# Kernel optimization log

Hardware: AMD Instinct MI355X
Metric: run time of the kernel (lower is better)

## Reference

```python
import jax, jax.numpy as jnp
import numpy as np

B, T, D = 2, 4096, 1024
H = 8
HD = D // H            # head_dim = 128
STRIDES = (1, 1, 2, 2, 4, 4, 8, 8)   # resolution_schedule
BANDS = 8              # spectral_bands
RH = 256               # router_hidden


def setup_inputs() -> dict:
    key = jax.random.key(0)
    ks = jax.random.split(key, 12)
    def xavier(k, shape):
        fan_in, fan_out = shape[-2], shape[-1]
        lim = 0.5 * (6.0 / (fan_in + fan_out)) ** 0.5   # gain=0.5 xavier_uniform
        return jax.random.uniform(k, shape, jnp.float32, -lim, lim)
    return {
        "x":          jax.random.normal(ks[0], (B, T, D), jnp.float32),
        "Wq":         xavier(ks[1], (H, D, HD)),
        "Wk":         xavier(ks[2], (H, D, HD)),
        "Wv":         xavier(ks[3], (H, D, HD)),
        "band_gates": jax.random.normal(ks[4], (H, BANDS), jnp.float32) * 0.1,
        "alphas":     jax.random.normal(ks[5], (H,), jnp.float32) * 0.1,
        "rW1":        xavier(ks[6], (D, RH)),
        "rb1":        jnp.zeros((RH,), jnp.float32),
        "rW2":        xavier(ks[7], (RH, H)),
        "rb2":        jnp.zeros((H,), jnp.float32),
        "Wout":       xavier(ks[8], (HD, D)),
    }


def _flux_head(x, Wq, Wk, Wv, band_gate, alpha, stride):
    # one FluxHead: strided K/V pooling + spectral logit gating + contra-flow residual
    q = jnp.einsum('btd,dh->bth', x, Wq)          # [B,T,HD]
    k = jnp.einsum('btd,dh->bth', x, Wk)
    v = jnp.einsum('btd,dh->bth', x, Wv)
    Tk = T // stride
    k = k.reshape(B, Tk, stride, HD).mean(axis=2)  # avg-pool K/V along time
    v = v.reshape(B, Tk, stride, HD).mean(axis=2)
    logits = jnp.einsum('bth,bkh->btk', q, k) / jnp.sqrt(jnp.float32(HD))  # [B,T,Tk]
    # spectral frequency gating on logits (rFFT over key axis, per-band sigmoid gain)
    F = jnp.fft.rfft(logits, axis=-1)              # [B,T,Tk//2+1] complex
    nbins = F.shape[-1]
    band_idx = jnp.clip((jnp.arange(nbins) * BANDS) // nbins, 0, BANDS - 1)
    gains = jax.nn.sigmoid(band_gate)[band_idx]    # [nbins]
    logits = jnp.fft.irfft(F * gains, n=Tk, axis=-1)
    attn = jax.nn.softmax(logits, axis=-1)
    out = jnp.einsum('btk,bkh->bth', attn, v)      # [B,T,HD]
    # contra-flow: reverse-sequence residual with learned gate
    return out + jnp.tanh(alpha) * out[:, ::-1, :]


def reference(x, Wq, Wk, Wv, band_gates, alphas, rW1, rb1, rW2, rb2, Wout):
    head_outs = [
        _flux_head(x, Wq[h], Wk[h], Wv[h], band_gates[h], alphas[h], STRIDES[h])
        for h in range(H)
    ]
    stacked = jnp.stack(head_outs, axis=2)                      # [B,T,H,HD]
    hid = jax.nn.relu(jnp.einsum('btd,dr->btr', x, rW1) + rb1)  # router MLP
    w = jax.nn.softmax(jnp.einsum('btr,rh->bth', hid, rW2) + rb2, axis=-1)
    mixed = jnp.einsum('bth,bthc->btc', w, stacked)             # [B,T,HD]
    return jnp.einsum('btc,cd->btd', mixed, Wout)               # [B,T,D]
```

## Files before the change

kernel.cpp:

```cpp
#include <hip/hip_runtime.h>
#include <hip/hip_bf16.h>

typedef __attribute__((ext_vector_type(8))) short short8;
typedef __attribute__((ext_vector_type(4))) short short4v;
typedef __attribute__((ext_vector_type(4))) float f32x4;
typedef unsigned short u16;

#define T_ 4096
#define D_ 1024
#define ISSL2E (0.08838834764831845f * 1.4426950408889634f)

__device__ __forceinline__ u16 f2bf(float f) {
  union { float f; unsigned u; } v; v.f = f;
  unsigned r = v.u + 0x7FFFu + ((v.u >> 16) & 1u);
  return (u16)(r >> 16);
}

__global__ __launch_bounds__(256) void prep_all(const float* __restrict__ x,
    const float* __restrict__ Wq, const float* __restrict__ Wk, const float* __restrict__ Wv,
    const float* __restrict__ rW1, const float* __restrict__ Wout,
    u16* __restrict__ p1, u16* __restrict__ p2, u16* __restrict__ p4, u16* __restrict__ p8,
    u16* __restrict__ wqT, u16* __restrict__ kvT, u16* __restrict__ rw1T, u16* __restrict__ woutT) {
  const int blk = blockIdx.x;
  if (blk < 1024) {
    const int b = blk >> 9, t0 = (blk & 511) << 3;
    const float* src = x + ((long)b * T_ + t0) * D_;
#pragma unroll
    for (int j = 0; j < 4; ++j) {
      const int c = threadIdx.x + j * 256;
      float v[8];
#pragma unroll
      for (int r = 0; r < 8; ++r) v[r] = src[r * D_ + c];
#pragma unroll
      for (int r = 0; r < 8; ++r) p1[((long)b * 4096 + t0 + r) * D_ + c] = f2bf(v[r]);
#pragma unroll
      for (int r = 0; r < 4; ++r)
        p2[((long)b * 2048 + (t0 >> 1) + r) * D_ + c] = f2bf((v[2*r] + v[2*r+1]) * 0.5f);
#pragma unroll
      for (int r = 0; r < 2; ++r)
        p4[((long)b * 1024 + (t0 >> 2) + r) * D_ + c] =
            f2bf((v[4*r] + v[4*r+1] + v[4*r+2] + v[4*r+3]) * 0.25f);
      p8[((long)b * 512 + (t0 >> 3)) * D_ + c] =
          f2bf((v[0]+v[1]+v[2]+v[3]+v[4]+v[5]+v[6]+v[7]) * 0.125f);
    }
    return;
  }
  const int idx = (blk - 1024) * 256 + threadIdx.x;
  if (idx < 1048576) {
    const int h = idx >> 17, wi = idx & 131071;
    const int c = wi >> 10, k = wi & 1023;
    wqT[idx] = f2bf(Wq[(long)h * 131072 + k * 128 + c]);
  } else if (idx < 3145728) {
    const int lid = idx - 1048576;
    const int g = lid >> 19, wi = lid & 524287;
    const int n = wi >> 10, k = wi & 1023;
    const int kv = n >> 8, hh = (n >> 7) & 1, c = n & 127;
    const float* W = kv ? Wv : Wk;
    kvT[lid] = f2bf(W[(long)(2 * g + hh) * 131072 + k * 128 + c]);
  } else if (idx < 3407872) {
    const int lid = idx - 3145728;
    const int n = lid >> 10, k = lid & 1023;
    rw1T[lid] = f2bf(rW1[(long)k * 256 + n]);
  } else if (idx < 3538944) {
    const int lid = idx - 3407872;
    const int n = lid >> 7, k = lid & 127;
    woutT[lid] = f2bf(Wout[(long)k * 1024 + n]);
  }
}

__global__ __launch_bounds__(256) void tpose_all(const u16* __restrict__ KV,
                                                 u16* __restrict__ KT, u16* __restrict__ VT) {
  const int xt = blockIdx.x;
  int g, lx;
  if (xt < 128)      { g = 0; lx = xt; }
  else if (xt < 192) { g = 1; lx = xt - 128; }
  else if (xt < 224) { g = 2; lx = xt - 192; }
  else               { g = 3; lx = xt - 224; }
  const int Tk = 4096 >> g;
  const long kvrow[4] = {0, 8192, 12288, 14336};
  const long ktoff[4] = {0, 2097152, 3145728, 3670016};
  __shared__ u16 tile[32][33];
  const int z = blockIdx.z;
  const int b = z & 1, hh = (z >> 1) & 1, kv = z >> 2;
  const u16* src = KV + kvrow[g] * 512 + (long)b * Tk * 512 + kv * 256 + hh * 128;
  u16* dst = (kv ? VT : KT) + ktoff[g] + (long)(hh * 2 + b) * 128 * Tk;
  const int r0 = lx * 32, c0 = blockIdx.y * 32;
  const int ci = threadIdx.x & 31, ri = threadIdx.x >> 5;
#pragma unroll
  for (int j = 0; j < 4; ++j)
    tile[ri + 8 * j][ci] = src[(long)(r0 + ri + 8 * j) * 512 + c0 + ci];
  __syncthreads();
  const int key = r0 + ci;
  const int col = kv ? ((key & ~63) | (((key >> 4) & 1) << 5) | (((key >> 2) & 3) << 3)
                                    | (((key >> 5) & 1) << 2) | (key & 3))
                     : key;
#pragma unroll
  for (int j = 0; j < 4; ++j)
    dst[(long)(c0 + ri + 8 * j) * Tk + col] = tile[ci][ri + 8 * j];
}

__global__ __launch_bounds__(256) void irfft_c(const float* __restrict__ bg, u16* __restrict__ crep) {
  const int h = blockIdx.y;
  const int Tk = 4096 >> (h >> 1);
  const int mask = Tk - 1;
  if ((int)(blockIdx.x * 256) >= Tk) return;
  const int nb = (Tk >> 1) + 1;
  __shared__ float ct[4096];
  __shared__ float wm[2049];
  const int tid = threadIdx.x;
  const float w0 = 6.283185307179586f / (float)Tk;
  for (int j = tid; j < Tk; j += 256) ct[j] = cosf(w0 * (float)j);
  for (int m = tid; m < nb; m += 256) {
    int band = (m * 8) / nb; if (band > 7) band = 7;
    const float g = 1.f / (1.f + expf(-bg[h * 8 + band]));
    const float sc = (m == 0 || m == nb - 1) ? 1.f : 2.f;
    wm[m] = g * sc / (float)Tk;
  }
  __syncthreads();
  const int n = blockIdx.x * 256 + tid;
  float acc = 0.f;
  int idx = 0;
  for (int m = 0; m < nb; ++m) {
    acc += wm[m] * ct[idx];
    idx += n;
    if (idx >= Tk) idx -= Tk;
  }
  const u16 bf = f2bf(acc);
  u16* hb = crep + (long)h * 16416;
#pragma unroll
  for (int p = 0; p < 4; ++p) {
    const int q = (n - p) & mask;
    hb[p * 4104 + q] = bf;
    if (q < 8) hb[p * 4104 + q + Tk] = bf;
  }
}

__device__ __forceinline__ void gll16(const void* g, void* l) {
  __builtin_amdgcn_global_load_lds((const __attribute__((address_space(1))) void*)g,
                                   (__attribute__((address_space(3))) void*)l, 16, 0, 0);
}

__device__ __forceinline__ void gemm_core(const u16* __restrict__ A, const u16* __restrict__ Bt,
    void* __restrict__ Cv, int K, int lda, int ldb, int ldc, int tm, int tn, float alpha,
    bool obf, u16 (*lds)[2][128][32]) {
  const int tid = threadIdx.x, lane = tid & 63, wid = tid >> 6;
  const int wr = wid >> 1, wc = wid & 1;
  const int srow = lane >> 2;
  const int scol = ((lane & 3) ^ ((lane >> 3) & 3)) * 8;
  const u16* ga0 = A + (long)(tm + 32 * wid + srow) * lda + scol;
  const u16* ga1 = ga0 + (long)16 * lda;
  const u16* gb0 = Bt + (long)(tn + 32 * wid + srow) * ldb + scol;
  const u16* gb1 = gb0 + (long)16 * ldb;
  f32x4 acc[4][4] = {};
  const int nk = K >> 5;
  gll16(ga0, &lds[0][0][32 * wid][0]);
  gll16(ga1, &lds[0][0][32 * wid + 16][0]);
  gll16(gb0, &lds[0][1][32 * wid][0]);
  gll16(gb1, &lds[0][1][32 * wid + 16][0]);
  int buf = 0;
  const int fr = lane & 15;
  const int fo2 = (((lane >> 4) & 3) ^ ((lane >> 1) & 3)) * 8;
  for (int kt = 0; kt < nk; ++kt) {
    __syncthreads();
    if (kt + 1 < nk) {
      const long ko = (long)(kt + 1) * 32;
      gll16(ga0 + ko, &lds[buf ^ 1][0][32 * wid][0]);
      gll16(ga1 + ko, &lds[buf ^ 1][0][32 * wid + 16][0]);
      gll16(gb0 + ko, &lds[buf ^ 1][1][32 * wid][0]);
      gll16(gb1 + ko, &lds[buf ^ 1][1][32 * wid + 16][0]);
    }
    short8 af[4], bfr[4];
#pragma unroll
    for (int i = 0; i < 4; ++i) {
      af[i]  = *(const short8*)&lds[buf][0][wr * 64 + i * 16 + fr][fo2];
      bfr[i] = *(const short8*)&lds[buf][1][wc * 64 + i * 16 + fr][fo2];
    }
#pragma unroll
    for (int i = 0; i < 4; ++i)
#pragma unroll
      for (int j = 0; j < 4; ++j)
        acc[i][j] = __builtin_amdgcn_mfma_f32_16x16x32_bf16(af[i], bfr[j], acc[i][j], 0, 0, 0);
    buf ^= 1;
  }
  const int er = (lane >> 4) * 4, ec = lane & 15;
  if (obf) {
    u16* C = (u16*)Cv;
#pragma unroll
    for (int i = 0; i < 4; ++i)
#pragma unroll
      for (int j = 0; j < 4; ++j)
#pragma unroll
        for (int r = 0; r < 4; ++r)
          C[(long)(tm + wr * 64 + i * 16 + er + r) * ldc + (tn + wc * 64 + j * 16 + ec)] =
              f2bf(acc[i][j][r] * alpha);
  } else {
    float* C = (float*)Cv;
#pragma unroll
    for (int i = 0; i < 4; ++i)
#pragma unroll
      for (int j = 0; j < 4; ++j)
#pragma unroll
        for (int r = 0; r < 4; ++r)
          C[(long)(tm + wr * 64 + i * 16 + er + r) * ldc + (tn + wc * 64 + j * 16 + ec)] =
              acc[i][j][r] * alpha;
  }
}

template <bool OBF>
__global__ __launch_bounds__(256) void gemm_bt(const u16* __restrict__ A, const u16* __restrict__ Bt,
                                               void* __restrict__ Cv, int K, int lda, int ldb, int ldc,
                                               long abs_, long bbs, long cbs, float alpha) {
  __shared__ u16 lds[2][2][128][32];
  const u16* Az = A + (long)blockIdx.z * abs_;
  const u16* Bz = Bt + (long)blockIdx.z * bbs;
  void* Cz = OBF ? (void*)((u16*)Cv + (long)blockIdx.z * cbs)
                 : (void*)((float*)Cv + (long)blockIdx.z * cbs);
  gemm_core(Az, Bz, Cz, K, lda, ldb, ldc, blockIdx.x * 128, blockIdx.y * 128, alpha, OBF, lds);
}

__global__ __launch_bounds__(256) void gemm_p1(const u16* __restrict__ xbf,
    const u16* __restrict__ wqT, const u16* __restrict__ kvT, const u16* __restrict__ rw1T,
    u16* __restrict__ Qb, u16* __restrict__ KV, float* __restrict__ hid) {
  __shared__ u16 lds[2][2][128][32];
  const int bid = blockIdx.x;
  const int id = (bid & 7) * 140 + (bid >> 3);
  if (id < 512) {
    gemm_core(xbf, wqT, Qb, 1024, 1024, 1024, 1024,
              (id >> 3) * 128, (id & 7) * 128, 1.f, true, lds);
  } else if (id < 992) {
    const int lid = id - 512;
    const int rt = lid >> 2, y = lid & 3;
    int g, lr;
    if (rt < 64)       { g = 0; lr = rt; }
    else if (rt < 96)  { g = 1; lr = rt - 64; }
    else if (rt < 112) { g = 2; lr = rt - 96; }
    else               { g = 3; lr = rt - 112; }
    const long xofs[4] = {0, 8388608, 12582912, 14680064};
    const long kvrow[4] = {0, 8192, 12288, 14336};
    gemm_core(xbf + xofs[g], kvT + (long)g * 524288, KV + kvrow[g] * 512,
              1024, 1024, 1024, 512, lr * 128, y * 128, 1.f, true, lds);
  } else {
    const int lid = id - 992;
    gemm_core(xbf, rw1T, hid, 1024, 1024, 1024, 256,
              (lid >> 1) * 128, (lid & 1) * 128, 1.f, false, lds);
  }
}

__global__ __launch_bounds__(256) void conv_k(const u16* __restrict__ crep,
    const u16* __restrict__ KT, u16* __restrict__ Kp) {
  const int z = blockIdx.z, h = z >> 1, b = z & 1, g = h >> 1;
  const int Tk = 4096 >> g, mask = Tk - 1;
  const int tm = blockIdx.x << 7;
  if (tm >= Tk) return;
  __shared__ u16 clds[16416];
  __shared__ u16 blds[2][4][128][32];
  const int tid = threadIdx.x, lane = tid & 63, wid = tid >> 6;
  const int wr = wid >> 1, wc = wid & 1;
  const int srow = lane >> 2;
  const int scol = ((lane & 3) ^ ((lane >> 3) & 3)) * 8;
  const int fr = lane & 15, fo = (lane >> 4) * 8;
  const int fo2 = (((lane >> 4) & 3) ^ ((lane >> 1) & 3)) * 8;
  {
    const short8* src = (const short8*)(crep + (long)h * 16416);
    short8* dst = (short8*)clds;
    for (int j = tid; j < 2052; j += 256) dst[j] = src[j];
  }
  const long ktofs = 4194304 - (4194304 >> g);
  const u16* Bt = KT + ktofs + (long)((h & 1) * 2 + b) * 128 * Tk;
  u16* out = Kp + ktofs + ((long)(h & 1) << 8) * Tk + ((long)b << 7) * Tk;
  const u16* gb0 = Bt + (long)(32 * wid + srow) * Tk + scol;
  const u16* gb1 = gb0 + (long)16 * Tk;
  f32x4 acc[4][4] = {};
  int base[4];
#pragma unroll
  for (int i = 0; i < 4; ++i) base[i] = (fo - (tm + wr * 64 + i * 16 + fr)) & mask;
  const int p = base[0] & 3;
  const u16* crow = clds + p * 4104;
  const int nk = Tk >> 7;
#pragma unroll
  for (int c = 0; c < 4; ++c) {
    gll16(gb0 + c * 32, &blds[0][c][32 * wid][0]);
    gll16(gb1 + c * 32, &blds[0][c][32 * wid + 16][0]);
  }
  int buf = 0;
  for (int kt = 0; kt < nk; ++kt) {
    __syncthreads();
    if (kt + 1 < nk) {
      const long ko = (long)(kt + 1) * 128;
#pragma unroll
      for (int c = 0; c < 4; ++c) {
        gll16(gb0 + ko + c * 32, &blds[buf ^ 1][c][32 * wid][0]);
        gll16(gb1 + ko + c * 32, &blds[buf ^ 1][c][32 * wid + 16][0]);
      }
    }
#pragma unroll
    for (int c = 0; c < 4; ++c) {
      short8 af[4], bfr[4];
#pragma unroll
      for (int i = 0; i < 4; ++i) {
        const int a0 = base[i] ^ p;
        short4v lo = *(const short4v*)(crow + a0);
        short4v hi = *(const short4v*)(crow + a0 + 4);
        af[i][0] = lo[0]; af[i][1] = lo[1]; af[i][2] = lo[2]; af[i][3] = lo[3];
        af[i][4] = hi[0]; af[i][5] = hi[1]; af[i][6] = hi[2]; af[i][7] = hi[3];
        base[i] = (base[i] + 32) & mask;
        bfr[i] = *(const short8*)&blds[buf][c][wc * 64 + i * 16 + fr][fo2];
      }
#pragma unroll
      for (int i = 0; i < 4; ++i)
#pragma unroll
        for (int j = 0; j < 4; ++j)
          acc[i][j] = __builtin_amdgcn_mfma_f32_16x16x32_bf16(af[i], bfr[j], acc[i][j], 0, 0, 0);
    }
    buf ^= 1;
  }
  const int er = (lane >> 4) * 4, ec = lane & 15;
#pragma unroll
  for (int i = 0; i < 4; ++i)
#pragma unroll
    for (int j = 0; j < 4; ++j)
#pragma unroll
      for (int r = 0; r < 4; ++r)
        out[(long)(tm + wr * 64 + i * 16 + er + r) * 128 + (wc * 64 + j * 16 + ec)] =
            f2bf(acc[i][j][r] * ISSL2E);
}

__global__ __launch_bounds__(256, 2) void flash(const u16* __restrict__ Qb,
    const u16* __restrict__ Kp, const u16* __restrict__ VT, float* __restrict__ O) {
  const int wg = blockIdx.x;
  const int x = wg & 7, s = wg >> 3;
  const int t4 = s >> 4;
  const int lvl = t4 ^ (t4 >> 1);
  const int hh = x >> 2, b = (x >> 1) & 1;
  const int h = lvl * 2 + hh;
  const int qtm = (((x & 1) << 4) + (s & 15)) << 7;
  const int Tk = 4096 >> lvl;
  const int nt = Tk >> 6;

  __shared__ __align__(16) char smem[65536];
  u16 (*Kl)[4][64][32] = (u16(*)[4][64][32])smem;
  u16 (*Vl)[128][64]   = (u16(*)[128][64])(smem + 32768);

  const int tid = threadIdx.x, lane = tid & 63, wid = tid >> 6;
  const int fr = lane & 15, gs = lane >> 4;
  const int fo = gs * 8;
  const int fo2 = ((gs & 3) ^ ((lane >> 1) & 3)) * 8;

  const long ktofs = 4194304 - (4194304 >> lvl);
  const u16* kbase = Kp + ktofs + (long)(hh * 2 + b) * 128 * Tk;
  const u16* vbase = VT + ktofs + (long)(hh * 2 + b) * 128 * Tk;

  short8 aq[2][4];
#pragma unroll
  for (int m = 0; m < 2; ++m)
#pragma unroll
    for (int kk = 0; kk < 4; ++kk)
      aq[m][kk] = *(const short8*)(Qb +
          ((long)(b * 4096 + qtm + wid * 32 + m * 16 + fr)) * 1024 + h * 128 + kk * 32 + fo);

  const u16* kptr = kbase + (long)(lane >> 2) * 128 + wid * 32 +
                    (((lane & 3) ^ ((lane >> 3) & 3)) << 3);
  const u16* vptr = vbase + (long)(32 * wid + (lane >> 3)) * Tk +
                    (((lane & 7) ^ ((lane >> 3) & 7)) << 3);

  const char* kbL  = smem + fr * 64 + fo2 * 2;
  const char* vbL0 = smem + 32768 + fr * 128 + ((((gs    ) ^ (fr & 7)) & 7) << 4);
  const char* vbL1 = smem + 32768 + fr * 128 + ((((gs ^ 4) ^ (fr & 7)) & 7) << 4);

  f32x4 acc[2][8] = {};
  f32x4 accl[2] = {};
  float mr[2] = {-3e38f, -3e38f};

  short8 ones;
#pragma unroll
  for (int i = 0; i < 8; ++i) ones[i] = (short)0x3F80;

#pragma unroll
  for (int i = 0; i < 4; ++i) {
    gll16(kptr + i * 2048, &Kl[0][wid][i * 16][0]);
    gll16(vptr + (long)i * 8 * Tk, &Vl[0][32 * wid + 8 * i][0]);
  }

  int cur = 0;
  for (int kt = 0; kt < nt; ++kt) {
    asm volatile("s_waitcnt vmcnt(0)" ::: "memory");
    __builtin_amdgcn_sched_barrier(0);
    __builtin_amdgcn_s_barrier();
    __builtin_amdgcn_sched_barrier(0);
    if (kt + 1 < nt) {
      const int ktn = kt + 1;
#pragma unroll
      for (int i = 0; i < 4; ++i) {
        gll16(kptr + (long)ktn * 8192 + i * 2048, &Kl[cur ^ 1][wid][i * 16][0]);
        gll16(vptr + (long)ktn * 64 + (long)i * 8 * Tk, &Vl[cur ^ 1][32 * wid + 8 * i][0]);
      }
    }
    const char* kc = kbL + cur * 16384;
    f32x4 sa[2][4] = {};
    __builtin_amdgcn_s_setprio(1);
#pragma unroll
    for (int kk = 0; kk < 4; ++kk) {
      short8 bk[4];
#pragma unroll
      for (int jm = 0; jm < 4; ++jm)
        bk[jm] = *(const short8*)(kc + kk * 4096 + jm * 1024);
#pragma unroll
      for (int m = 0; m < 2; ++m)
#pragma unroll
        for (int jm = 0; jm < 4; ++jm)
          sa[m][jm] = __builtin_amdgcn_mfma_f32_16x16x32_bf16(bk[jm], aq[m][kk], sa[m][jm], 0, 0, 0);
    }
    __builtin_amdgcn_s_setprio(0);
    float tmx[2];
#pragma unroll
    for (int m = 0; m < 2; ++m) {
      float v0 = fmaxf(fmaxf(sa[m][0][0], sa[m][0][1]), fmaxf(sa[m][0][2], sa[m][0][3]));
      float v1 = fmaxf(fmaxf(sa[m][1][0], sa[m][1][1]), fmaxf(sa[m][1][2], sa[m][1][3]));
      float v2 = fmaxf(fmaxf(sa[m][2][0], sa[m][2][1]), fmaxf(sa[m][2][2], sa[m][2][3]));
      float v3 = fmaxf(fmaxf(sa[m][3][0], sa[m][3][1]), fmaxf(sa[m][3][2], sa[m][3][3]));
      float v = fmaxf(fmaxf(v0, v1), fmaxf(v2, v3));
      v = fmaxf(v, __shfl_xor(v, 16));
      v = fmaxf(v, __shfl_xor(v, 32));
      tmx[m] = v;
    }
    const bool need = (tmx[0] > mr[0] + 8.f) | (tmx[1] > mr[1] + 8.f);
    if (__any((int)need)) {
#pragma unroll
      for (int m = 0; m < 2; ++m) {
        const float mn = fmaxf(mr[m], tmx[m]);
        const float av = __builtin_amdgcn_exp2f(mr[m] - mn);
        mr[m] = mn;
#pragma unroll
        for (int jd = 0; jd < 8; ++jd)
#pragma unroll
          for (int r = 0; r < 4; ++r) acc[m][jd][r] *= av;
#pragma unroll
        for (int r = 0; r < 4; ++r) accl[m][r] *= av;
      }
    }
#pragma unroll
    for (int m = 0; m < 2; ++m)
#pragma unroll
      for (int jm = 0; jm < 4; ++jm)
#pragma unroll
        for (int r = 0; r < 4; ++r)
          sa[m][jm][r] = __builtin_amdgcn_exp2f(sa[m][jm][r] - mr[m]);
    unsigned pk[2][4][2];
#pragma unroll
    for (int m = 0; m < 2; ++m)
#pragma unroll
      for (int jm = 0; jm < 4; ++jm) {
        asm("v_cvt_pk_bf16_f32 %0, %1, %2" : "=v"(pk[m][jm][0]) : "v"(sa[m][jm][0]), "v"(sa[m][jm][1]));
        asm("v_cvt_pk_bf16_f32 %0, %1, %2" : "=v"(pk[m][jm][1]) : "v"(sa[m][jm][2]), "v"(sa[m][jm][3]));
      }
    const char* vc0 = vbL0 + cur * 16384;
    const char* vc1 = vbL1 + cur * 16384;
    __builtin_amdgcn_s_setprio(1);
#pragma unroll
    for (int kk = 0; kk < 2; ++kk) {
      short8 pt[2];
#pragma unroll
      for (int m = 0; m < 2; ++m) {
        union { unsigned u[4]; short8 s; } pp;
        pp.u[0] = pk[m][kk][0];     pp.u[1] = pk[m][kk][1];
        pp.u[2] = pk[m][kk + 2][0]; pp.u[3] = pk[m][kk + 2][1];
        pt[m] = pp.s;
      }
      const char* vc = kk ? vc1 : vc0;
#pragma unroll
      for (int jd = 0; jd < 8; ++jd) {
        short8 bb = *(const short8*)(vc + jd * 2048);
#pragma unroll
        for (int m = 0; m < 2; ++m)
          acc[m][jd] = __builtin_amdgcn_mfma_f32_16x16x32_bf16(bb, pt[m], acc[m][jd], 0, 0, 0);
      }
#pragma unroll
      for (int m = 0; m < 2; ++m)
        accl[m] = __builtin_amdgcn_mfma_f32_16x16x32_bf16(ones, pt[m], accl[m], 0, 0, 0);
    }
    __builtin_amdgcn_s_setprio(0);
    cur ^= 1;
  }
  __syncthreads();
  float* Ot = (float*)smem;
  float* ot = Ot + wid * 16 * 132;
#pragma unroll
  for (int m = 0; m < 2; ++m) {
    const float inv = 1.f / accl[m][0];
#pragma unroll
    for (int jd = 0; jd < 8; ++jd) {
      f32x4 v;
#pragma unroll
      for (int r = 0; r < 4; ++r) v[r] = acc[m][jd][r] * inv;
      *(f32x4*)&ot[fr * 132 + jd * 16 + gs * 4] = v;
    }
    asm volatile("s_waitcnt lgkmcnt(0)" ::: "memory");
    __builtin_amdgcn_sched_barrier(0);
    const int q = qtm + wid * 32 + m * 16 + (lane >> 2);
    float* od = O + ((long)(b * 4096 + q) * 8 + h) * 128 + (lane & 3) * 32;
#pragma unroll
    for (int j = 0; j < 8; ++j) {
      f32x4 v = *(const f32x4*)&ot[(lane >> 2) * 132 + (lane & 3) * 32 + j * 4];
      *(f32x4*)&od[j * 4] = v;
    }
    asm volatile("s_waitcnt lgkmcnt(0)" ::: "memory");
    __builtin_amdgcn_sched_barrier(0);
  }
}

__global__ __launch_bounds__(256) void router_mix(const float* __restrict__ hid,
    const float* __restrict__ rb1, const float* __restrict__ rW2, const float* __restrict__ rb2,
    const float* __restrict__ al, const float* __restrict__ O, u16* __restrict__ mixed) {
  const int tok = blockIdx.x;
  const int b = tok >> 12, t = tok & 4095;
  const int tid = threadIdx.x;
  __shared__ float lred[4][8];
  __shared__ float wgt[8];
  __shared__ float ta[8];
  const float hv = fmaxf(hid[(long)tok * 256 + tid] + rb1[tid], 0.f);
  const float4* w4 = (const float4*)(rW2 + tid * 8);
  const float4 wa = w4[0], wb = w4[1];
  float part[8] = {hv * wa.x, hv * wa.y, hv * wa.z, hv * wa.w,
                   hv * wb.x, hv * wb.y, hv * wb.z, hv * wb.w};
#pragma unroll
  for (int h = 0; h < 8; ++h) {
    float v = part[h];
#pragma unroll
    for (int o = 1; o < 64; o <<= 1) v += __shfl_xor(v, o);
    if ((tid & 63) == 0) lred[tid >> 6][h] = v;
  }
  __syncthreads();
  if (tid < 8) ta[tid] = tanhf(al[tid]);
  if (tid == 0) {
    float lg[8], m = -1e30f;
#pragma unroll
    for (int h = 0; h < 8; ++h) {
      lg[h] = lred[0][h] + lred[1][h] + lred[2][h] + lred[3][h] + rb2[h];
      m = fmaxf(m, lg[h]);
    }
    float s = 0.f;
#pragma unroll
    for (int h = 0; h < 8; ++h) { lg[h] = __expf(lg[h] - m); s += lg[h]; }
    const float inv = 1.f / s;
#pragma unroll
    for (int h = 0; h < 8; ++h) wgt[h] = lg[h] * inv;
  }
  __syncthreads();
  if (tid < 128) {
    const long base = (long)tok * 1024 + tid;
    const long rbase = ((long)b * 4096 + (4095 - t)) * 1024 + tid;
    float acc = 0.f;
#pragma unroll
    for (int h = 0; h < 8; ++h)
      acc += wgt[h] * (O[base + h * 128] + ta[h] * O[rbase + h * 128]);
    mixed[(long)tok * 128 + tid] = f2bf(acc);
  }
}

extern "C" void kernel_launch(void* const* d_in, const int* in_sizes, int n_in,
                              void* d_out, int out_size, void* d_ws, size_t ws_size,
                              hipStream_t stream) {
  const float* x    = (const float*)d_in[0];
  const float* Wq   = (const float*)d_in[1];
  const float* Wk   = (const float*)d_in[2];
  const float* Wv   = (const float*)d_in[3];
  const float* bg   = (const float*)d_in[4];
  const float* al   = (const float*)d_in[5];
  const float* rW1  = (const float*)d_in[6];
  const float* rb1  = (const float*)d_in[7];
  const float* rW2  = (const float*)d_in[8];
  const float* rb2  = (const float*)d_in[9];
  const float* Wout = (const float*)d_in[10];
  float* out = (float*)d_out;

  const size_t MB = 1u << 20;
  char* w = (char*)d_ws;
  u16*   xbf   = (u16*)(w + 0);
  float* O     = (float*)(w + 0);
  u16*   Qb    = (u16*)(w + 32 * MB);
  u16*   KV    = (u16*)(w + 48 * MB);
  u16*   Kp    = (u16*)(w + 48 * MB);
  u16*   KT    = (u16*)(w + 63 * MB);
  u16*   VT    = (u16*)(w + 70 * MB + 512 * 1024);
  float* hid   = (float*)(w + 78 * MB);
  u16*   wqT   = (u16*)(w + 86 * MB);
  u16*   kvT   = (u16*)(w + 88 * MB);
  u16*   rw1T  = (u16*)(w + 92 * MB);
  u16*   woutT = (u16*)(w + 92 * MB + 512 * 1024);
  u16*   crep  = (u16*)(w + 92 * MB + 768 * 1024);
  u16*   mixed = (u16*)(w + 93 * MB + 512 * 1024);
  u16*   xp2   = (u16*)(w + 16 * MB);
  u16*   xp4   = (u16*)(w + 24 * MB);
  u16*   xp8   = (u16*)(w + 28 * MB);

  prep_all<<<dim3(14848), dim3(256), 0, stream>>>(x, Wq, Wk, Wv, rW1, Wout,
      xbf, xp2, xp4, xp8, wqT, kvT, rw1T, woutT);

  gemm_p1<<<dim3(1120), dim3(256), 0, stream>>>(xbf, wqT, kvT, rw1T, Qb, KV, hid);

  tpose_all<<<dim3(240, 4, 8), dim3(256), 0, stream>>>(KV, KT, VT);
  irfft_c<<<dim3(16, 8), dim3(256), 0, stream>>>(bg, crep);

  conv_k<<<dim3(32, 1, 16), dim3(256), 0, stream>>>(crep, KT, Kp);

  flash<<<dim3(512), dim3(256), 0, stream>>>(Qb, Kp, VT, O);

  router_mix<<<dim3(8192), dim3(256), 0, stream>>>(hid, rb1, rW2, rb2, al, O, mixed);
  gemm_bt<false><<<dim3(64, 8), dim3(256), 0, stream>>>(mixed, woutT, out,
      128, 128, 128, 1024, 0, 0, 0, 1.f);
}
```

Measured before the change: 320.9 us.

## Single-buffer V tile in flash for higher occupancy; fold irfft into prep

```diff
diff --git a/kernel.cpp b/kernel.cpp
--- a/kernel.cpp
+++ b/kernel.cpp
@@ -18,16 +18,18 @@
 
 __global__ __launch_bounds__(256) void prep_all(const float* __restrict__ x,
     const float* __restrict__ Wq, const float* __restrict__ Wk, const float* __restrict__ Wv,
-    const float* __restrict__ rW1, const float* __restrict__ Wout,
+    const float* __restrict__ rW1, const float* __restrict__ Wout, const float* __restrict__ bg,
     u16* __restrict__ p1, u16* __restrict__ p2, u16* __restrict__ p4, u16* __restrict__ p8,
-    u16* __restrict__ wqT, u16* __restrict__ kvT, u16* __restrict__ rw1T, u16* __restrict__ woutT) {
+    u16* __restrict__ wqT, u16* __restrict__ kvT, u16* __restrict__ rw1T, u16* __restrict__ woutT,
+    u16* __restrict__ crep) {
   const int blk = blockIdx.x;
+  const int tid = threadIdx.x;
   if (blk < 1024) {
     const int b = blk >> 9, t0 = (blk & 511) << 3;
     const float* src = x + ((long)b * T_ + t0) * D_;
 #pragma unroll
     for (int j = 0; j < 4; ++j) {
-      const int c = threadIdx.x + j * 256;
+      const int c = tid + j * 256;
       float v[8];
 #pragma unroll
       for (int r = 0; r < 8; ++r) v[r] = src[r * D_ + c];
@@ -45,26 +47,62 @@
     }
     return;
   }
-  const int idx = (blk - 1024) * 256 + threadIdx.x;
-  if (idx < 1048576) {
-    const int h = idx >> 17, wi = idx & 131071;
-    const int c = wi >> 10, k = wi & 1023;
-    wqT[idx] = f2bf(Wq[(long)h * 131072 + k * 128 + c]);
-  } else if (idx < 3145728) {
-    const int lid = idx - 1048576;
-    const int g = lid >> 19, wi = lid & 524287;
-    const int n = wi >> 10, k = wi & 1023;
-    const int kv = n >> 8, hh = (n >> 7) & 1, c = n & 127;
-    const float* W = kv ? Wv : Wk;
-    kvT[lid] = f2bf(W[(long)(2 * g + hh) * 131072 + k * 128 + c]);
-  } else if (idx < 3407872) {
-    const int lid = idx - 3145728;
-    const int n = lid >> 10, k = lid & 1023;
-    rw1T[lid] = f2bf(rW1[(long)k * 256 + n]);
-  } else if (idx < 3538944) {
-    const int lid = idx - 3407872;
-    const int n = lid >> 7, k = lid & 127;
-    woutT[lid] = f2bf(Wout[(long)k * 1024 + n]);
+  if (blk < 14848) {
+    const int idx = (blk - 1024) * 256 + tid;
+    if (idx < 1048576) {
+      const int h = idx >> 17, wi = idx & 131071;
+      const int c = wi >> 10, k = wi & 1023;
+      wqT[idx] = f2bf(Wq[(long)h * 131072 + k * 128 + c]);
+    } else if (idx < 3145728) {
+      const int lid = idx - 1048576;
+      const int g = lid >> 19, wi = lid & 524287;
+      const int n = wi >> 10, k = wi & 1023;
+      const int kv = n >> 8, hh = (n >> 7) & 1, c = n & 127;
+      const float* W = kv ? Wv : Wk;
+      kvT[lid] = f2bf(W[(long)(2 * g + hh) * 131072 + k * 128 + c]);
+    } else if (idx < 3407872) {
+      const int lid = idx - 3145728;
+      const int n = lid >> 10, k = lid & 1023;
+      rw1T[lid] = f2bf(rW1[(long)k * 256 + n]);
+    } else if (idx < 3538944) {
+      const int lid = idx - 3407872;
+      const int n = lid >> 7, k = lid & 127;
+      woutT[lid] = f2bf(Wout[(long)k * 1024 + n]);
+    }
+    return;
+  }
+  const int rel = blk - 14848;
+  const int h = rel >> 4, xi = rel & 15;
+  const int Tk = 4096 >> (h >> 1);
+  const int mask = Tk - 1;
+  if (xi * 256 >= Tk) return;
+  const int nb = (Tk >> 1) + 1;
+  __shared__ float ct[4096];
+  __shared__ float wm[2049];
+  const float w0 = 6.283185307179586f / (float)Tk;
+  for (int j = tid; j < Tk; j += 256) ct[j] = cosf(w0 * (float)j);
+  for (int m = tid; m < nb; m += 256) {
+    int band = (m * 8) / nb; if (band > 7) band = 7;
+    const float g = 1.f / (1.f + expf(-bg[h * 8 + band]));
+    const float sc = (m == 0 || m == nb - 1) ? 1.f : 2.f;
+    wm[m] = g * sc / (float)Tk;
+  }
+  __syncthreads();
+  const int n = xi * 256 + tid;
+  float acc = 0.f;
+  int idx = 0;
+  for (int m = 0; m < nb; ++m) {
+    acc += wm[m] * ct[idx];
+    idx += n;
+    if (idx >= Tk) idx -= Tk;
+  }
+  const u16 bf = f2bf(acc);
+  u16* hb = crep + (long)h * 16416;
+#pragma unroll
+  for (int p = 0; p < 4; ++p) {
+    const int q = (n - p) & mask;
+    hb[p * 4104 + q] = bf;
+    if (q < 8) hb[p * 4104 + q + Tk] = bf;
   }
 }
 
@@ -97,42 +135,6 @@
 #pragma unroll
   for (int j = 0; j < 4; ++j)
     dst[(long)(c0 + ri + 8 * j) * Tk + col] = tile[ci][ri + 8 * j];
-}
-
-__global__ __launch_bounds__(256) void irfft_c(const float* __restrict__ bg, u16* __restrict__ crep) {
-  const int h = blockIdx.y;
-  const int Tk = 4096 >> (h >> 1);
-  const int mask = Tk - 1;
-  if ((int)(blockIdx.x * 256) >= Tk) return;
-  const int nb = (Tk >> 1) + 1;
-  __shared__ float ct[4096];
-  __shared__ float wm[2049];
-  const int tid = threadIdx.x;
-  const float w0 = 6.283185307179586f / (float)Tk;
-  for (int j = tid; j < Tk; j += 256) ct[j] = cosf(w0 * (float)j);
-  for (int m = tid; m < nb; m += 256) {
-    int band = (m * 8) / nb; if (band > 7) band = 7;
-    const float g = 1.f / (1.f + expf(-bg[h * 8 + band]));
-    const float sc = (m == 0 || m == nb - 1) ? 1.f : 2.f;
-    wm[m] = g * sc / (float)Tk;
-  }
-  __syncthreads();
-  const int n = blockIdx.x * 256 + tid;
-  float acc = 0.f;
-  int idx = 0;
-  for (int m = 0; m < nb; ++m) {
-    acc += wm[m] * ct[idx];
-    idx += n;
-    if (idx >= Tk) idx -= Tk;
-  }
-  const u16 bf = f2bf(acc);
-  u16* hb = crep + (long)h * 16416;
-#pragma unroll
-  for (int p = 0; p < 4; ++p) {
-    const int q = (n - p) & mask;
-    hb[p * 4104 + q] = bf;
-    if (q < 8) hb[p * 4104 + q + Tk] = bf;
-  }
 }
 
 __device__ __forceinline__ void gll16(const void* g, void* l) {
@@ -325,7 +327,7 @@
             f2bf(acc[i][j][r] * ISSL2E);
 }
 
-__global__ __launch_bounds__(256, 2) void flash(const u16* __restrict__ Qb,
+__global__ __launch_bounds__(256, 3) void flash(const u16* __restrict__ Qb,
     const u16* __restrict__ Kp, const u16* __restrict__ VT, float* __restrict__ O) {
   const int wg = blockIdx.x;
   const int x = wg & 7, s = wg >> 3;
@@ -337,9 +339,9 @@
   const int Tk = 4096 >> lvl;
   const int nt = Tk >> 6;
 
-  __shared__ __align__(16) char smem[65536];
+  __shared__ __align__(16) char smem[49152];
   u16 (*Kl)[4][64][32] = (u16(*)[4][64][32])smem;
-  u16 (*Vl)[128][64]   = (u16(*)[128][64])(smem + 32768);
+  u16 (*Vl)[64]        = (u16(*)[64])(smem + 32768);
 
   const int tid = threadIdx.x, lane = tid & 63, wid = tid >> 6;
   const int fr = lane & 15, gs = lane >> 4;
@@ -376,10 +378,7 @@
   for (int i = 0; i < 8; ++i) ones[i] = (short)0x3F80;
 
 #pragma unroll
-  for (int i = 0; i < 4; ++i) {
-    gll16(kptr + i * 2048, &Kl[0][wid][i * 16][0]);
-    gll16(vptr + (long)i * 8 * Tk, &Vl[0][32 * wid + 8 * i][0]);
-  }
+  for (int i = 0; i < 4; ++i) gll16(kptr + i * 2048, &Kl[0][wid][i * 16][0]);
 
   int cur = 0;
   for (int kt = 0; kt < nt; ++kt) {
@@ -387,13 +386,13 @@
     __builtin_amdgcn_sched_barrier(0);
     __builtin_amdgcn_s_barrier();
     __builtin_amdgcn_sched_barrier(0);
+#pragma unroll
+    for (int i = 0; i < 4; ++i)
+      gll16(vptr + (long)kt * 64 + (long)i * 8 * Tk, &Vl[32 * wid + 8 * i][0]);
     if (kt + 1 < nt) {
-      const int ktn = kt + 1;
-#pragma unroll
-      for (int i = 0; i < 4; ++i) {
-        gll16(kptr + (long)ktn * 8192 + i * 2048, &Kl[cur ^ 1][wid][i * 16][0]);
-        gll16(vptr + (long)ktn * 64 + (long)i * 8 * Tk, &Vl[cur ^ 1][32 * wid + 8 * i][0]);
-      }
+#pragma unroll
+      for (int i = 0; i < 4; ++i)
+        gll16(kptr + (long)(kt + 1) * 8192 + i * 2048, &Kl[cur ^ 1][wid][i * 16][0]);
     }
     const char* kc = kbL + cur * 16384;
     f32x4 sa[2][4] = {};
@@ -453,8 +452,11 @@
         asm("v_cvt_pk_bf16_f32 %0, %1, %2" : "=v"(pk[m][jm][0]) : "v"(sa[m][jm][0]), "v"(sa[m][jm][1]));
         asm("v_cvt_pk_bf16_f32 %0, %1, %2" : "=v"(pk[m][jm][1]) : "v"(sa[m][jm][2]), "v"(sa[m][jm][3]));
       }
-    const char* vc0 = vbL0 + cur * 16384;
-    const char* vc1 = vbL1 + cur * 16384;
+    if (kt + 1 < nt) { asm volatile("s_waitcnt vmcnt(4)" ::: "memory"); }
+    else             { asm volatile("s_waitcnt vmcnt(0)" ::: "memory"); }
+    __builtin_amdgcn_sched_barrier(0);
+    __builtin_amdgcn_s_barrier();
+    __builtin_amdgcn_sched_barrier(0);
     __builtin_amdgcn_s_setprio(1);
 #pragma unroll
     for (int kk = 0; kk < 2; ++kk) {
@@ -466,7 +468,7 @@
         pp.u[2] = pk[m][kk + 2][0]; pp.u[3] = pk[m][kk + 2][1];
         pt[m] = pp.s;
       }
-      const char* vc = kk ? vc1 : vc0;
+      const char* vc = kk ? vbL1 : vbL0;
 #pragma unroll
       for (int jd = 0; jd < 8; ++jd) {
         short8 bb = *(const short8*)(vc + jd * 2048);
@@ -593,13 +595,12 @@
   u16*   xp4   = (u16*)(w + 24 * MB);
   u16*   xp8   = (u16*)(w + 28 * MB);
 
-  prep_all<<<dim3(14848), dim3(256), 0, stream>>>(x, Wq, Wk, Wv, rW1, Wout,
-      xbf, xp2, xp4, xp8, wqT, kvT, rw1T, woutT);
+  prep_all<<<dim3(14976), dim3(256), 0, stream>>>(x, Wq, Wk, Wv, rW1, Wout, bg,
+      xbf, xp2, xp4, xp8, wqT, kvT, rw1T, woutT, crep);
 
   gemm_p1<<<dim3(1120), dim3(256), 0, stream>>>(xbf, wqT, kvT, rw1T, Qb, KV, hid);
 
   tpose_all<<<dim3(240, 4, 8), dim3(256), 0, stream>>>(KV, KT, VT);
-  irfft_c<<<dim3(16, 8), dim3(256), 0, stream>>>(bg, crep);
 
   conv_k<<<dim3(32, 1, 16), dim3(256), 0, stream>>>(crep, KT, Kp);
 
```

Measured after the change: 382.2 us. +19.1%, slower.
